# Optimization experiments

Measured on AMD Instinct MI355X. Metric: run time of the kernel, lower is better.

The kernel has to match this reference:

```python
import jax, jax.numpy as jnp
import numpy as np

B, S, D = 2, 2048, 1024
H, DH = 16, 64
INNER = H * DH  # 1024
FF = 4 * D
WINDOW = 128
EPS = 1e-5
SCALE = DH ** -0.5


def setup_inputs() -> dict:
    key = jax.random.key(0)
    ks = jax.random.split(key, 8)
    s = lambda fan_in: 1.0 / np.sqrt(fan_in)
    return {
        "x": jax.random.normal(ks[0], (B, S, D), dtype=jnp.float32),
        "ln1_g": jnp.ones((D,), jnp.float32),
        "ln1_b": jnp.zeros((D,), jnp.float32),
        "w_qkv": jax.random.uniform(ks[1], (3 * INNER, D), jnp.float32, -s(D), s(D)),
        "w_out": jax.random.uniform(ks[2], (D, INNER), jnp.float32, -s(INNER), s(INNER)),
        "b_out": jnp.zeros((D,), jnp.float32),
        "ln2_g": jnp.ones((D,), jnp.float32),
        "ln2_b": jnp.zeros((D,), jnp.float32),
        "w_ff1": jax.random.uniform(ks[3], (FF, D), jnp.float32, -s(D), s(D)),
        "b_ff1": jnp.zeros((FF,), jnp.float32),
        "w_ff2": jax.random.uniform(ks[4], (D, FF), jnp.float32, -s(FF), s(FF)),
        "b_ff2": jnp.zeros((D,), jnp.float32),
    }


def _layernorm(x, g, b):
    mu = jnp.mean(x, axis=-1, keepdims=True)
    var = jnp.mean(jnp.square(x - mu), axis=-1, keepdims=True)
    return (x - mu) * jax.lax.rsqrt(var + EPS) * g + b


def reference(x, ln1_g, ln1_b, w_qkv, w_out, b_out, ln2_g, ln2_b, w_ff1, b_ff1, w_ff2, b_ff2):
    # --- attention block ---
    residual = x
    h = _layernorm(x, ln1_g, ln1_b)
    qkv = h @ w_qkv.T                             # [B, S, 3*INNER]
    q, k, v = jnp.split(qkv, 3, axis=-1)
    reshape_heads = lambda t: t.reshape(B, S, H, DH).transpose(0, 2, 1, 3)  # [B,H,S,DH]
    q, k, v = map(reshape_heads, (q, k, v))
    q = q * SCALE
    scores = jnp.einsum("bhqd,bhkd->bhqk", q, k)  # dense [B,H,S,S]
    # local sparse pattern: attend iff |i-j| <= window_size
    idx = jnp.arange(S)
    local_mask = jnp.abs(idx[:, None] - idx[None, :]) <= WINDOW  # [S,S] bool
    scores = jnp.where(local_mask[None, None], scores, -jnp.inf)
    attn = jax.nn.softmax(scores, axis=-1)
    attn = jnp.nan_to_num(attn, nan=0.0)
    out = jnp.einsum("bhqk,bhkd->bhqd", attn, v)  # [B,H,S,DH]
    out = out.transpose(0, 2, 1, 3).reshape(B, S, INNER)
    out = out @ w_out.T + b_out                   # dropout inactive (eval)
    x = residual + out
    # --- FFN block ---
    residual = x
    h = _layernorm(x, ln2_g, ln2_b)
    h = jax.nn.gelu(h @ w_ff1.T + b_ff1, approximate=False)
    h = h @ w_ff2.T + b_ff2
    return residual + h
```

## Files before the change

### kernel.cpp

```cpp
#include <hip/hip_runtime.h>
#include <stdint.h>

#define SEQ    2048
#define NB     2
#define DMODEL 1024
#define NHEAD  16
#define HDIM   64
#define FFDIM  4096
#define WIN    128
#define MTOK   (NB*SEQ)

typedef short short8 __attribute__((ext_vector_type(8)));
typedef float f32x4  __attribute__((ext_vector_type(4)));

__device__ __forceinline__ float bf2f(uint16_t h){ return __uint_as_float(((uint32_t)h) << 16); }
__device__ __forceinline__ uint16_t f2bf(float f){
  uint32_t u = __float_as_uint(f);
  u += 0x7fffu + ((u >> 16) & 1u);
  return (uint16_t)(u >> 16);
}

__device__ __forceinline__ float gelu_f(float v){
  float u = 0.7978845608028654f * v * (1.0f + 0.044715f * v * v);
  u = fminf(fmaxf(u, -10.0f), 10.0f);
  const float e = __expf(2.0f * u);
  const float th = (e - 1.0f) / (e + 1.0f);
  return 0.5f * v * (1.0f + th);
}

__device__ __forceinline__ void gl_lds16(const void* g, void* l) {
  __builtin_amdgcn_global_load_lds((const __attribute__((address_space(1))) void*)g,
                                   (__attribute__((address_space(3))) void*)l, 16, 0, 0);
}

__global__ __launch_bounds__(256) void cvt4_kernel(
    const float* __restrict__ s0, const float* __restrict__ s1,
    const float* __restrict__ s2, const float* __restrict__ s3,
    uint16_t* __restrict__ d0, uint16_t* __restrict__ d1,
    uint16_t* __restrict__ d2, uint16_t* __restrict__ d3)
{
  size_t i = (size_t)blockIdx.x * 256 + threadIdx.x;
  const float* s; uint16_t* d; size_t off;
  if      (i <  768*1024) { s = s0; d = d0; off = i; }
  else if (i < 1024*1024) { s = s1; d = d1; off = i -  768*1024; }
  else if (i < 2048*1024) { s = s2; d = d2; off = i - 1024*1024; }
  else                    { s = s3; d = d3; off = i - 2048*1024; }
  const float4 v = ((const float4*)s)[off];
  uint2 o;
  o.x = (uint32_t)f2bf(v.x) | ((uint32_t)f2bf(v.y) << 16);
  o.y = (uint32_t)f2bf(v.z) | ((uint32_t)f2bf(v.w) << 16);
  ((uint2*)d)[off] = o;
}

__global__ __launch_bounds__(256) void ln_kernel(const float* __restrict__ x,
                                                 const float* __restrict__ g,
                                                 const float* __restrict__ b,
                                                 uint16_t* __restrict__ y)
{
  const int row = blockIdx.x;
  const int t = threadIdx.x;
  const float4 v = ((const float4*)(x + (size_t)row * DMODEL))[t];
  float s1 = v.x + v.y + v.z + v.w;
  float s2 = v.x*v.x + v.y*v.y + v.z*v.z + v.w*v.w;
  #pragma unroll
  for (int off = 32; off; off >>= 1) { s1 += __shfl_xor(s1, off, 64); s2 += __shfl_xor(s2, off, 64); }
  __shared__ float red[8];
  const int w = t >> 6;
  if ((t & 63) == 0) { red[w] = s1; red[4+w] = s2; }
  __syncthreads();
  s1 = red[0]+red[1]+red[2]+red[3];
  s2 = red[4]+red[5]+red[6]+red[7];
  const float mu = s1 * (1.0f/DMODEL);
  const float var = s2 * (1.0f/DMODEL) - mu*mu;
  const float rs = rsqrtf(var + 1e-5f);
  const float4 gv = ((const float4*)g)[t];
  const float4 bv = ((const float4*)b)[t];
  uint2 o;
  o.x = (uint32_t)f2bf((v.x-mu)*rs*gv.x + bv.x) | ((uint32_t)f2bf((v.y-mu)*rs*gv.y + bv.y) << 16);
  o.y = (uint32_t)f2bf((v.z-mu)*rs*gv.z + bv.z) | ((uint32_t)f2bf((v.w-mu)*rs*gv.w + bv.w) << 16);
  ((uint2*)(y + (size_t)row * DMODEL))[t] = o;
}


template<int EPI>
__global__ __launch_bounds__(256) void gemm_bt(
    const uint16_t* __restrict__ A, const uint16_t* __restrict__ Bm,
    const float* __restrict__ bias, uint16_t* __restrict__ C,
    int M, int N, int K)
{
  __shared__ __align__(16) uint16_t As[128*64];
  __shared__ __align__(16) uint16_t Bs[128*64];
  const int t = threadIdx.x;
  const int l = t & 63;
  const int w = t >> 6;
  const int row0 = blockIdx.y * 128;
  const int col0 = blockIdx.x * 128;
  const int wm = (w >> 1) * 64, wn = (w & 1) * 64;

  f32x4 acc[4][4];
  #pragma unroll
  for (int i = 0; i < 4; ++i)
    #pragma unroll
    for (int j = 0; j < 4; ++j)
      #pragma unroll
      for (int e = 0; e < 4; ++e) acc[i][j][e] = 0.0f;

  const int sr8 = t >> 3;
  const int sg  = (t & 7) ^ (sr8 & 7);
  const uint16_t* aG = A  + (size_t)(row0 + sr8) * K + sg * 8;
  const uint16_t* bG = Bm + (size_t)(col0 + sr8) * K + sg * 8;
  char* aL = (char*)As + t * 16;
  char* bL = (char*)Bs + t * 16;
  const int mrow = l & 15;
  const int kq = l >> 4;

  for (int k0 = 0; k0 < K; k0 += 64) {
    #pragma unroll
    for (int c = 0; c < 4; ++c) {
      gl_lds16(aG + k0 + (size_t)(c*32) * K, aL + c*4096);
      gl_lds16(bG + k0 + (size_t)(c*32) * K, bL + c*4096);
    }
    __syncthreads();
    #pragma unroll
    for (int ks = 0; ks < 2; ++ks) {
      const int pa = ((ks*4 + kq) ^ (mrow & 7)) * 16;
      short8 af[4], bfr[4];
      #pragma unroll
      for (int mi = 0; mi < 4; ++mi)
        af[mi] = *(const short8*)((const char*)As + (wm + mi*16 + mrow) * 128 + pa);
      #pragma unroll
      for (int ni = 0; ni < 4; ++ni)
        bfr[ni] = *(const short8*)((const char*)Bs + (wn + ni*16 + mrow) * 128 + pa);
      #pragma unroll
      for (int mi = 0; mi < 4; ++mi)
        #pragma unroll
        for (int ni = 0; ni < 4; ++ni)
          acc[mi][ni] = __builtin_amdgcn_mfma_f32_16x16x32_bf16(af[mi], bfr[ni], acc[mi][ni], 0, 0, 0);
    }
    __syncthreads();
  }

  const int crow = (l >> 4) * 4;
  float bv[4];
  #pragma unroll
  for (int ni = 0; ni < 4; ++ni)
    bv[ni] = (EPI != 0) ? bias[col0 + wn + ni*16 + mrow] : 0.0f;
  #pragma unroll
  for (int mi = 0; mi < 4; ++mi) {
    #pragma unroll
    for (int r = 0; r < 4; ++r) {
      const int row = row0 + wm + mi*16 + crow + r;
      #pragma unroll
      for (int ni = 0; ni < 4; ++ni) {
        const int col = col0 + wn + ni*16 + mrow;
        float v = acc[mi][ni][r] + bv[ni];
        if (EPI == 2) v = gelu_f(v);
        C[(size_t)row * N + col] = f2bf(v);
      }
    }
  }
}

__global__ __launch_bounds__(256) void gemm_sk64(
    const uint16_t* __restrict__ A, const uint16_t* __restrict__ Bm,
    float* __restrict__ P0, float* __restrict__ P1,
    int M, int N, int K, int KS)
{
  __shared__ __align__(16) uint16_t As[128*64];
  __shared__ __align__(16) uint16_t Bs[64*64];
  const int t = threadIdx.x;
  const int l = t & 63;
  const int w = t >> 6;
  const int row0 = blockIdx.y * 128;
  const int col0 = blockIdx.x * 64;
  const int kbase = blockIdx.z * KS;
  float* P = blockIdx.z ? P1 : P0;
  const int wm = (w >> 1) * 64, wn = (w & 1) * 32;

  f32x4 acc[4][2];
  #pragma unroll
  for (int i = 0; i < 4; ++i)
    #pragma unroll
    for (int j = 0; j < 2; ++j)
      #pragma unroll
      for (int e = 0; e < 4; ++e) acc[i][j][e] = 0.0f;

  const int sr8 = t >> 3;
  const int sg  = (t & 7) ^ (sr8 & 7);
  const uint16_t* aG = A  + (size_t)(row0 + sr8) * K + kbase + sg * 8;
  const uint16_t* bG = Bm + (size_t)(col0 + sr8) * K + kbase + sg * 8;
  char* aL = (char*)As + t * 16;
  char* bL = (char*)Bs + t * 16;
  const int mrow = l & 15;
  const int kq = l >> 4;

  for (int k0 = 0; k0 < KS; k0 += 64) {
    #pragma unroll
    for (int c = 0; c < 4; ++c)
      gl_lds16(aG + k0 + (size_t)(c*32) * K, aL + c*4096);
    #pragma unroll
    for (int c = 0; c < 2; ++c)
      gl_lds16(bG + k0 + (size_t)(c*32) * K, bL + c*4096);
    __syncthreads();
    #pragma unroll
    for (int ks = 0; ks < 2; ++ks) {
      const int pa = ((ks*4 + kq) ^ (mrow & 7)) * 16;
      short8 af[4], bfr[2];
      #pragma unroll
      for (int mi = 0; mi < 4; ++mi)
        af[mi] = *(const short8*)((const char*)As + (wm + mi*16 + mrow) * 128 + pa);
      #pragma unroll
      for (int ni = 0; ni < 2; ++ni)
        bfr[ni] = *(const short8*)((const char*)Bs + (wn + ni*16 + mrow) * 128 + pa);
      #pragma unroll
      for (int mi = 0; mi < 4; ++mi)
        #pragma unroll
        for (int ni = 0; ni < 2; ++ni)
          acc[mi][ni] = __builtin_amdgcn_mfma_f32_16x16x32_bf16(af[mi], bfr[ni], acc[mi][ni], 0, 0, 0);
    }
    __syncthreads();
  }

  const int crow = (l >> 4) * 4;
  #pragma unroll
  for (int mi = 0; mi < 4; ++mi)
    #pragma unroll
    for (int r = 0; r < 4; ++r) {
      const int row = row0 + wm + mi*16 + crow + r;
      #pragma unroll
      for (int ni = 0; ni < 2; ++ni)
        P[(size_t)row * N + col0 + wn + ni*16 + mrow] = acc[mi][ni][r];
    }
}

__global__ __launch_bounds__(256) void gemm_sk128(
    const uint16_t* __restrict__ A, const uint16_t* __restrict__ Bm,
    uint16_t* __restrict__ P0, uint16_t* __restrict__ P1,
    uint16_t* __restrict__ P2, uint16_t* __restrict__ P3,
    int M, int N, int K, int KS)
{
  __shared__ __align__(16) uint16_t As[128*64];
  __shared__ __align__(16) uint16_t Bs[128*64];
  const int t = threadIdx.x;
  const int l = t & 63;
  const int w = t >> 6;
  const int row0 = blockIdx.y * 128;
  const int col0 = blockIdx.x * 128;
  const int z = blockIdx.z;
  const int kbase = z * KS;
  uint16_t* P = (z < 2) ? (z ? P1 : P0) : (z == 2 ? P2 : P3);
  const int wm = (w >> 1) * 64, wn = (w & 1) * 64;

  f32x4 acc[4][4];
  #pragma unroll
  for (int i = 0; i < 4; ++i)
    #pragma unroll
    for (int j = 0; j < 4; ++j)
      #pragma unroll
      for (int e = 0; e < 4; ++e) acc[i][j][e] = 0.0f;

  const int sr8 = t >> 3;
  const int sg  = (t & 7) ^ (sr8 & 7);
  const uint16_t* aG = A  + (size_t)(row0 + sr8) * K + kbase + sg * 8;
  const uint16_t* bG = Bm + (size_t)(col0 + sr8) * K + kbase + sg * 8;
  char* aL = (char*)As + t * 16;
  char* bL = (char*)Bs + t * 16;
  const int mrow = l & 15;
  const int kq = l >> 4;

  for (int k0 = 0; k0 < KS; k0 += 64) {
    #pragma unroll
    for (int c = 0; c < 4; ++c) {
      gl_lds16(aG + k0 + (size_t)(c*32) * K, aL + c*4096);
      gl_lds16(bG + k0 + (size_t)(c*32) * K, bL + c*4096);
    }
    __syncthreads();
    #pragma unroll
    for (int ks = 0; ks < 2; ++ks) {
      const int pa = ((ks*4 + kq) ^ (mrow & 7)) * 16;
      short8 af[4], bfr[4];
      #pragma unroll
      for (int mi = 0; mi < 4; ++mi)
        af[mi] = *(const short8*)((const char*)As + (wm + mi*16 + mrow) * 128 + pa);
      #pragma unroll
      for (int ni = 0; ni < 4; ++ni)
        bfr[ni] = *(const short8*)((const char*)Bs + (wn + ni*16 + mrow) * 128 + pa);
      #pragma unroll
      for (int mi = 0; mi < 4; ++mi)
        #pragma unroll
        for (int ni = 0; ni < 4; ++ni)
          acc[mi][ni] = __builtin_amdgcn_mfma_f32_16x16x32_bf16(af[mi], bfr[ni], acc[mi][ni], 0, 0, 0);
    }
    __syncthreads();
  }

  const int crow = (l >> 4) * 4;
  #pragma unroll
  for (int mi = 0; mi < 4; ++mi)
    #pragma unroll
    for (int r = 0; r < 4; ++r) {
      const int row = row0 + wm + mi*16 + crow + r;
      #pragma unroll
      for (int ni = 0; ni < 4; ++ni)
        P[(size_t)row * N + col0 + wn + ni*16 + mrow] = f2bf(acc[mi][ni][r]);
    }
}

__global__ __launch_bounds__(256) void combine_ln2_kernel(
    const float* __restrict__ p0, const float* __restrict__ p1,
    const float* __restrict__ x,  const float* __restrict__ bout,
    const float* __restrict__ g,  const float* __restrict__ b,
    float* __restrict__ X2f, uint16_t* __restrict__ H2)
{
  const int row = blockIdx.x;
  const int t = threadIdx.x;
  const size_t off = (size_t)row * (DMODEL/4) + t;
  const float4 a0 = ((const float4*)p0)[off];
  const float4 a1 = ((const float4*)p1)[off];
  const float4 xv = ((const float4*)x)[off];
  const float4 bo = ((const float4*)bout)[t];
  float4 v;
  v.x = a0.x + a1.x + xv.x + bo.x;
  v.y = a0.y + a1.y + xv.y + bo.y;
  v.z = a0.z + a1.z + xv.z + bo.z;
  v.w = a0.w + a1.w + xv.w + bo.w;
  ((float4*)X2f)[off] = v;
  float s1 = v.x + v.y + v.z + v.w;
  float s2 = v.x*v.x + v.y*v.y + v.z*v.z + v.w*v.w;
  #pragma unroll
  for (int o = 32; o; o >>= 1) { s1 += __shfl_xor(s1, o, 64); s2 += __shfl_xor(s2, o, 64); }
  __shared__ float red[8];
  const int w = t >> 6;
  if ((t & 63) == 0) { red[w] = s1; red[4+w] = s2; }
  __syncthreads();
  s1 = red[0]+red[1]+red[2]+red[3];
  s2 = red[4]+red[5]+red[6]+red[7];
  const float mu = s1 * (1.0f/DMODEL);
  const float var = s2 * (1.0f/DMODEL) - mu*mu;
  const float rs = rsqrtf(var + 1e-5f);
  const float4 gv = ((const float4*)g)[t];
  const float4 bv = ((const float4*)b)[t];
  uint2 o;
  o.x = (uint32_t)f2bf((v.x-mu)*rs*gv.x + bv.x) | ((uint32_t)f2bf((v.y-mu)*rs*gv.y + bv.y) << 16);
  o.y = (uint32_t)f2bf((v.z-mu)*rs*gv.z + bv.z) | ((uint32_t)f2bf((v.w-mu)*rs*gv.w + bv.w) << 16);
  ((uint2*)(H2 + (size_t)row * DMODEL))[t] = o;
}

__global__ __launch_bounds__(256) void combine_ff2_kernel(
    const uint16_t* __restrict__ p0, const uint16_t* __restrict__ p1,
    const uint16_t* __restrict__ p2, const uint16_t* __restrict__ p3,
    const float* __restrict__ bff2, const float* __restrict__ X2f,
    float* __restrict__ out)
{
  const int row = blockIdx.x;
  const int t = threadIdx.x;
  const size_t eoff = (size_t)row * DMODEL + t * 4;
  const uint2 u0 = *(const uint2*)(p0 + eoff);
  const uint2 u1 = *(const uint2*)(p1 + eoff);
  const uint2 u2 = *(const uint2*)(p2 + eoff);
  const uint2 u3 = *(const uint2*)(p3 + eoff);
  const float4 xv = ((const float4*)X2f)[(size_t)row * (DMODEL/4) + t];
  const float4 bo = ((const float4*)bff2)[t];
  float4 v;
  v.x = bf2f((uint16_t)(u0.x & 0xffff)) + bf2f((uint16_t)(u1.x & 0xffff))
      + bf2f((uint16_t)(u2.x & 0xffff)) + bf2f((uint16_t)(u3.x & 0xffff)) + bo.x + xv.x;
  v.y = bf2f((uint16_t)(u0.x >> 16)) + bf2f((uint16_t)(u1.x >> 16))
      + bf2f((uint16_t)(u2.x >> 16)) + bf2f((uint16_t)(u3.x >> 16)) + bo.y + xv.y;
  v.z = bf2f((uint16_t)(u0.y & 0xffff)) + bf2f((uint16_t)(u1.y & 0xffff))
      + bf2f((uint16_t)(u2.y & 0xffff)) + bf2f((uint16_t)(u3.y & 0xffff)) + bo.z + xv.z;
  v.w = bf2f((uint16_t)(u0.y >> 16)) + bf2f((uint16_t)(u1.y >> 16))
      + bf2f((uint16_t)(u2.y >> 16)) + bf2f((uint16_t)(u3.y >> 16)) + bo.w + xv.w;
  ((float4*)out)[(size_t)row * (DMODEL/4) + t] = v;
}

#define TQ    32
#define NKT   18
#define NKP   (NKT*16)
#define KSTR  72
#define PSTR  296

__global__ __launch_bounds__(256) void attn_kernel(const uint16_t* __restrict__ qkv,
                                                   uint16_t* __restrict__ out)
{
  __shared__ uint16_t Qs[TQ * KSTR];
  __shared__ uint16_t Ps[TQ * PSTR];
  __shared__ uint16_t KV[NKP * KSTR];
  const int t = threadIdx.x, l = t & 63, w = t >> 6;
  const int b = blockIdx.z, hh = blockIdx.y, q0 = blockIdx.x * TQ;
  const int k0 = (q0 - WIN > 0) ? (q0 - WIN) : 0;
  const int kend_ = q0 + TQ + WIN;
  const int kend = (kend_ < SEQ) ? kend_ : SEQ;
  const int nk = kend - k0;

  {
    const int r = t >> 3, gg = t & 7;
    const uint4 qv = *(const uint4*)(qkv + (size_t)(b*SEQ + q0 + r) * 3072 + hh*64 + gg*8);
    *(uint4*)((char*)Qs + r*(KSTR*2) + gg*16) = qv;
    for (int j = r; j < NKP; j += 32) {
      uint4 kv; kv.x = 0; kv.y = 0; kv.z = 0; kv.w = 0;
      if (j < nk)
        kv = *(const uint4*)(qkv + (size_t)(b*SEQ + k0 + j) * 3072 + 1024 + hh*64 + gg*8);
      *(uint4*)((char*)KV + j*(KSTR*2) + gg*16) = kv;
    }
  }
  __syncthreads();

  if (w < 2) {
    const int rb = w * 16;
    const int mrow = l & 15, q4 = l >> 4;
    const short8 aq0 = *(const short8*)((const char*)Qs + (rb + mrow)*(KSTR*2) + q4*16);
    const short8 aq1 = *(const short8*)((const char*)Qs + (rb + mrow)*(KSTR*2) + 64 + q4*16);
    f32x4 cacc[NKT];
    #pragma unroll
    for (int ct = 0; ct < NKT; ++ct) {
      f32x4 c; c[0]=0.f; c[1]=0.f; c[2]=0.f; c[3]=0.f;
      const short8 b0 = *(const short8*)((const char*)KV + (ct*16 + mrow)*(KSTR*2) + q4*16);
      const short8 b1 = *(const short8*)((const char*)KV + (ct*16 + mrow)*(KSTR*2) + 64 + q4*16);
      c = __builtin_amdgcn_mfma_f32_16x16x32_bf16(aq0, b0, c, 0, 0, 0);
      c = __builtin_amdgcn_mfma_f32_16x16x32_bf16(aq1, b1, c, 0, 0, 0);
      cacc[ct] = c;
    }
    #pragma unroll
    for (int r = 0; r < 4; ++r) {
      const int iq = q0 + rb + q4*4 + r;
      float m = -1e30f;
      #pragma unroll
      for (int ct = 0; ct < NKT; ++ct) {
        const int jj = ct*16 + mrow;
        const int j = k0 + jj;
        const bool ok = (jj < nk) && (j >= iq - WIN) && (j <= iq + WIN);
        const float s = ok ? cacc[ct][r] * 0.125f : -1e30f;
        cacc[ct][r] = s;
        m = fmaxf(m, s);
      }
      m = fmaxf(m, __shfl_xor(m, 1, 64));
      m = fmaxf(m, __shfl_xor(m, 2, 64));
      m = fmaxf(m, __shfl_xor(m, 4, 64));
      m = fmaxf(m, __shfl_xor(m, 8, 64));
      float s = 0.f;
      #pragma unroll
      for (int ct = 0; ct < NKT; ++ct) {
        const float e = __expf(cacc[ct][r] - m);
        cacc[ct][r] = e;
        s += e;
      }
      s += __shfl_xor(s, 1, 64);
      s += __shfl_xor(s, 2, 64);
      s += __shfl_xor(s, 4, 64);
      s += __shfl_xor(s, 8, 64);
      const float rinv = 1.0f / s;
      #pragma unroll
      for (int ct = 0; ct < NKT; ++ct)
        Ps[(rb + q4*4 + r) * PSTR + ct*16 + mrow] = f2bf(cacc[ct][r] * rinv);
    }
  }
  __syncthreads();

  {
    uint16_t* Vt = KV;
    const int gg = t & 7;
    for (int j = t >> 3; j < NKP; j += 32) {
      if (j < nk) {
        const uint4 v = *(const uint4*)(qkv + (size_t)(b*SEQ + k0 + j) * 3072 + 2048 + hh*64 + gg*8);
        uint16_t e[8] = { (uint16_t)(v.x & 0xffff), (uint16_t)(v.x >> 16),
                          (uint16_t)(v.y & 0xffff), (uint16_t)(v.y >> 16),
                          (uint16_t)(v.z & 0xffff), (uint16_t)(v.z >> 16),
                          (uint16_t)(v.w & 0xffff), (uint16_t)(v.w >> 16) };
        #pragma unroll
        for (int dd = 0; dd < 8; ++dd) Vt[(gg*8 + dd) * PSTR + j] = e[dd];
      } else {
        #pragma unroll
        for (int dd = 0; dd < 8; ++dd) Vt[(gg*8 + dd) * PSTR + j] = 0;
      }
    }
  }
  __syncthreads();

  {
    const uint16_t* Vt = KV;
    const int mrow = l & 15, q4 = l >> 4;
    const int rt = w & 1, dt0 = (w >> 1) * 2;
    f32x4 o0, o1;
    #pragma unroll
    for (int e = 0; e < 4; ++e) { o0[e] = 0.f; o1[e] = 0.f; }
    #pragma unroll
    for (int ks = 0; ks < 9; ++ks) {
      const short8 a  = *(const short8*)((const char*)Ps + (rt*16 + mrow)*(PSTR*2) + ks*64 + q4*16);
      const short8 v0 = *(const short8*)((const char*)Vt + ((dt0  )*16 + mrow)*(PSTR*2) + ks*64 + q4*16);
      const short8 v1 = *(const short8*)((const char*)Vt + ((dt0+1)*16 + mrow)*(PSTR*2) + ks*64 + q4*16);
      o0 = __builtin_amdgcn_mfma_f32_16x16x32_bf16(a, v0, o0, 0, 0, 0);
      o1 = __builtin_amdgcn_mfma_f32_16x16x32_bf16(a, v1, o1, 0, 0, 0);
    }
    #pragma unroll
    for (int r = 0; r < 4; ++r) {
      const int iq = q0 + rt*16 + q4*4 + r;
      const size_t rowoff = (size_t)(b*SEQ + iq) * DMODEL + hh*64;
      out[rowoff + (dt0  )*16 + mrow] = f2bf(o0[r]);
      out[rowoff + (dt0+1)*16 + mrow] = f2bf(o1[r]);
    }
  }
}

extern "C" void kernel_launch(void* const* d_in, const int* in_sizes, int n_in,
                              void* d_out, int out_size, void* d_ws, size_t ws_size,
                              hipStream_t stream)
{
  const float* x    = (const float*)d_in[0];
  const float* ln1g = (const float*)d_in[1];
  const float* ln1b = (const float*)d_in[2];
  const float* wqkv = (const float*)d_in[3];
  const float* wout = (const float*)d_in[4];
  const float* bout = (const float*)d_in[5];
  const float* ln2g = (const float*)d_in[6];
  const float* ln2b = (const float*)d_in[7];
  const float* wff1 = (const float*)d_in[8];
  const float* bff1 = (const float*)d_in[9];
  const float* wff2 = (const float*)d_in[10];
  const float* bff2 = (const float*)d_in[11];
  float* out = (float*)d_out;

  char* ws = (char*)d_ws;
  const size_t MB = (size_t)1 << 20;
  uint16_t* Wqkv = (uint16_t*)(ws);
  uint16_t* Wout = (uint16_t*)(ws +  6*MB);
  uint16_t* Wff1 = (uint16_t*)(ws +  8*MB);
  uint16_t* Wff2 = (uint16_t*)(ws + 16*MB);
  uint16_t* QKV  = (uint16_t*)(ws + 24*MB);
  uint16_t* H1   = (uint16_t*)(ws + 48*MB);
  uint16_t* AT   = H1;
  float*    X2f  = (float*)   (ws + 56*MB);
  uint16_t* H2   = (uint16_t*)(ws + 72*MB);
  float*    OP0  = (float*)   (ws + 24*MB);
  float*    OP1  = (float*)   (ws + 80*MB);
  uint16_t* FF1  = (uint16_t*)(ws + 24*MB);
  uint16_t* FP0  = (uint16_t*)(ws);
  uint16_t* FP1  = (uint16_t*)(ws +  8*MB);
  uint16_t* FP2  = (uint16_t*)(ws + 72*MB);
  uint16_t* FP3  = (uint16_t*)(ws + 80*MB);

  cvt4_kernel<<<12288, 256, 0, stream>>>(wqkv, wout, wff1, wff2, Wqkv, Wout, Wff1, Wff2);
  ln_kernel<<<MTOK, 256, 0, stream>>>(x, ln1g, ln1b, H1);
  gemm_bt<0><<<dim3(3072/128, MTOK/128), 256, 0, stream>>>(H1, Wqkv, nullptr, QKV, MTOK, 3072, DMODEL);
  attn_kernel<<<dim3(SEQ/TQ, NHEAD, NB), 256, 0, stream>>>(QKV, AT);
  gemm_sk64<<<dim3(DMODEL/64, MTOK/128, 2), 256, 0, stream>>>(AT, Wout, OP0, OP1, MTOK, DMODEL, DMODEL, DMODEL/2);
  combine_ln2_kernel<<<MTOK, 256, 0, stream>>>(OP0, OP1, x, bout, ln2g, ln2b, X2f, H2);
  gemm_bt<2><<<dim3(FFDIM/128, MTOK/128), 256, 0, stream>>>(H2, Wff1, bff1, FF1, MTOK, FFDIM, DMODEL);
  gemm_sk128<<<dim3(DMODEL/128, MTOK/128, 4), 256, 0, stream>>>(FF1, Wff2, FP0, FP1, FP2, FP3, MTOK, DMODEL, FFDIM, FFDIM/4);
  combine_ff2_kernel<<<MTOK, 256, 0, stream>>>(FP0, FP1, FP2, FP3, bff2, X2f, out);
}
```

Baseline: 367.2 us.

## Replace split-K GEMMs with 64x64 tiles and fused bias-residual epilogues

Folds the first layernorm into the weight-conversion kernel so one launch does both. The QKV projection moves to a 128x64 tile GEMM, which gives more blocks. The out-projection and FF2 split-K GEMMs and their combine kernels are replaced by a 64x64-tile GEMM that adds bias and residual directly in its epilogue, removing the partial-sum buffers and the extra passes over them. Layernorm 2 becomes a separate kernel. The trade-off is lower per-block reuse, and the FF2 GEMM now runs the full K=4096 in each block instead of splitting it.

```diff
diff --git a/kernel.cpp b/kernel.cpp
--- a/kernel.cpp
+++ b/kernel.cpp
@@ -33,23 +33,50 @@
                                    (__attribute__((address_space(3))) void*)l, 16, 0, 0);
 }
 
-__global__ __launch_bounds__(256) void cvt4_kernel(
+__global__ __launch_bounds__(256) void cvtln_kernel(
     const float* __restrict__ s0, const float* __restrict__ s1,
     const float* __restrict__ s2, const float* __restrict__ s3,
     uint16_t* __restrict__ d0, uint16_t* __restrict__ d1,
-    uint16_t* __restrict__ d2, uint16_t* __restrict__ d3)
-{
-  size_t i = (size_t)blockIdx.x * 256 + threadIdx.x;
-  const float* s; uint16_t* d; size_t off;
-  if      (i <  768*1024) { s = s0; d = d0; off = i; }
-  else if (i < 1024*1024) { s = s1; d = d1; off = i -  768*1024; }
-  else if (i < 2048*1024) { s = s2; d = d2; off = i - 1024*1024; }
-  else                    { s = s3; d = d3; off = i - 2048*1024; }
-  const float4 v = ((const float4*)s)[off];
-  uint2 o;
-  o.x = (uint32_t)f2bf(v.x) | ((uint32_t)f2bf(v.y) << 16);
-  o.y = (uint32_t)f2bf(v.z) | ((uint32_t)f2bf(v.w) << 16);
-  ((uint2*)d)[off] = o;
+    uint16_t* __restrict__ d2, uint16_t* __restrict__ d3,
+    const float* __restrict__ x, const float* __restrict__ g,
+    const float* __restrict__ b, uint16_t* __restrict__ y)
+{
+  __shared__ float red[8];
+  const int t = threadIdx.x;
+  if (blockIdx.x < 12288) {
+    size_t i = (size_t)blockIdx.x * 256 + t;
+    const float* s; uint16_t* d; size_t off;
+    if      (i <  768*1024) { s = s0; d = d0; off = i; }
+    else if (i < 1024*1024) { s = s1; d = d1; off = i -  768*1024; }
+    else if (i < 2048*1024) { s = s2; d = d2; off = i - 1024*1024; }
+    else                    { s = s3; d = d3; off = i - 2048*1024; }
+    const float4 v = ((const float4*)s)[off];
+    uint2 o;
+    o.x = (uint32_t)f2bf(v.x) | ((uint32_t)f2bf(v.y) << 16);
+    o.y = (uint32_t)f2bf(v.z) | ((uint32_t)f2bf(v.w) << 16);
+    ((uint2*)d)[off] = o;
+  } else {
+    const int row = blockIdx.x - 12288;
+    const float4 v = ((const float4*)(x + (size_t)row * DMODEL))[t];
+    float s1 = v.x + v.y + v.z + v.w;
+    float s2 = v.x*v.x + v.y*v.y + v.z*v.z + v.w*v.w;
+    #pragma unroll
+    for (int off = 32; off; off >>= 1) { s1 += __shfl_xor(s1, off, 64); s2 += __shfl_xor(s2, off, 64); }
+    const int w = t >> 6;
+    if ((t & 63) == 0) { red[w] = s1; red[4+w] = s2; }
+    __syncthreads();
+    s1 = red[0]+red[1]+red[2]+red[3];
+    s2 = red[4]+red[5]+red[6]+red[7];
+    const float mu = s1 * (1.0f/DMODEL);
+    const float var = s2 * (1.0f/DMODEL) - mu*mu;
+    const float rs = rsqrtf(var + 1e-5f);
+    const float4 gv = ((const float4*)g)[t];
+    const float4 bv = ((const float4*)b)[t];
+    uint2 o;
+    o.x = (uint32_t)f2bf((v.x-mu)*rs*gv.x + bv.x) | ((uint32_t)f2bf((v.y-mu)*rs*gv.y + bv.y) << 16);
+    o.y = (uint32_t)f2bf((v.z-mu)*rs*gv.z + bv.z) | ((uint32_t)f2bf((v.w-mu)*rs*gv.w + bv.w) << 16);
+    ((uint2*)(y + (size_t)row * DMODEL))[t] = o;
+  }
 }
 
 __global__ __launch_bounds__(256) void ln_kernel(const float* __restrict__ x,
@@ -161,10 +188,9 @@
   }
 }
 
-__global__ __launch_bounds__(256) void gemm_sk64(
+__global__ __launch_bounds__(256) void gemm_qkv(
     const uint16_t* __restrict__ A, const uint16_t* __restrict__ Bm,
-    float* __restrict__ P0, float* __restrict__ P1,
-    int M, int N, int K, int KS)
+    uint16_t* __restrict__ C, int M, int N, int K)
 {
   __shared__ __align__(16) uint16_t As[128*64];
   __shared__ __align__(16) uint16_t Bs[64*64];
@@ -173,8 +199,6 @@
   const int w = t >> 6;
   const int row0 = blockIdx.y * 128;
   const int col0 = blockIdx.x * 64;
-  const int kbase = blockIdx.z * KS;
-  float* P = blockIdx.z ? P1 : P0;
   const int wm = (w >> 1) * 64, wn = (w & 1) * 32;
 
   f32x4 acc[4][2];
@@ -187,14 +211,14 @@
 
   const int sr8 = t >> 3;
   const int sg  = (t & 7) ^ (sr8 & 7);
-  const uint16_t* aG = A  + (size_t)(row0 + sr8) * K + kbase + sg * 8;
-  const uint16_t* bG = Bm + (size_t)(col0 + sr8) * K + kbase + sg * 8;
+  const uint16_t* aG = A  + (size_t)(row0 + sr8) * K + sg * 8;
+  const uint16_t* bG = Bm + (size_t)(col0 + sr8) * K + sg * 8;
   char* aL = (char*)As + t * 16;
   char* bL = (char*)Bs + t * 16;
   const int mrow = l & 15;
   const int kq = l >> 4;
 
-  for (int k0 = 0; k0 < KS; k0 += 64) {
+  for (int k0 = 0; k0 < K; k0 += 64) {
     #pragma unroll
     for (int c = 0; c < 4; ++c)
       gl_lds16(aG + k0 + (size_t)(c*32) * K, aL + c*4096);
@@ -229,148 +253,82 @@
       const int row = row0 + wm + mi*16 + crow + r;
       #pragma unroll
       for (int ni = 0; ni < 2; ++ni)
-        P[(size_t)row * N + col0 + wn + ni*16 + mrow] = acc[mi][ni][r];
-    }
-}
-
-__global__ __launch_bounds__(256) void gemm_sk128(
+        C[(size_t)row * N + col0 + wn + ni*16 + mrow] = f2bf(acc[mi][ni][r]);
+    }
+}
+
+__global__ __launch_bounds__(256) void gemm64(
     const uint16_t* __restrict__ A, const uint16_t* __restrict__ Bm,
-    uint16_t* __restrict__ P0, uint16_t* __restrict__ P1,
-    uint16_t* __restrict__ P2, uint16_t* __restrict__ P3,
-    int M, int N, int K, int KS)
-{
-  __shared__ __align__(16) uint16_t As[128*64];
-  __shared__ __align__(16) uint16_t Bs[128*64];
+    const float* __restrict__ bias, const float* __restrict__ res,
+    float* __restrict__ out, int M, int N, int K)
+{
+  __shared__ __align__(16) uint16_t As[64*64];
+  __shared__ __align__(16) uint16_t Bs[64*64];
   const int t = threadIdx.x;
   const int l = t & 63;
   const int w = t >> 6;
-  const int row0 = blockIdx.y * 128;
-  const int col0 = blockIdx.x * 128;
-  const int z = blockIdx.z;
-  const int kbase = z * KS;
-  uint16_t* P = (z < 2) ? (z ? P1 : P0) : (z == 2 ? P2 : P3);
-  const int wm = (w >> 1) * 64, wn = (w & 1) * 64;
-
-  f32x4 acc[4][4];
-  #pragma unroll
-  for (int i = 0; i < 4; ++i)
-    #pragma unroll
-    for (int j = 0; j < 4; ++j)
+  const int row0 = blockIdx.y * 64;
+  const int col0 = blockIdx.x * 64;
+  const int wm = (w >> 1) * 32, wn = (w & 1) * 32;
+
+  f32x4 acc[2][2];
+  #pragma unroll
+  for (int i = 0; i < 2; ++i)
+    #pragma unroll
+    for (int j = 0; j < 2; ++j)
       #pragma unroll
       for (int e = 0; e < 4; ++e) acc[i][j][e] = 0.0f;
 
   const int sr8 = t >> 3;
   const int sg  = (t & 7) ^ (sr8 & 7);
-  const uint16_t* aG = A  + (size_t)(row0 + sr8) * K + kbase + sg * 8;
-  const uint16_t* bG = Bm + (size_t)(col0 + sr8) * K + kbase + sg * 8;
+  const uint16_t* aG = A  + (size_t)(row0 + sr8) * K + sg * 8;
+  const uint16_t* bG = Bm + (size_t)(col0 + sr8) * K + sg * 8;
   char* aL = (char*)As + t * 16;
   char* bL = (char*)Bs + t * 16;
   const int mrow = l & 15;
   const int kq = l >> 4;
 
-  for (int k0 = 0; k0 < KS; k0 += 64) {
-    #pragma unroll
-    for (int c = 0; c < 4; ++c) {
-      gl_lds16(aG + k0 + (size_t)(c*32) * K, aL + c*4096);
-      gl_lds16(bG + k0 + (size_t)(c*32) * K, bL + c*4096);
-    }
+  for (int k0 = 0; k0 < K; k0 += 64) {
+    gl_lds16(aG + k0,                    aL);
+    gl_lds16(aG + k0 + (size_t)32 * K,   aL + 4096);
+    gl_lds16(bG + k0,                    bL);
+    gl_lds16(bG + k0 + (size_t)32 * K,   bL + 4096);
     __syncthreads();
     #pragma unroll
     for (int ks = 0; ks < 2; ++ks) {
       const int pa = ((ks*4 + kq) ^ (mrow & 7)) * 16;
-      short8 af[4], bfr[4];
-      #pragma unroll
-      for (int mi = 0; mi < 4; ++mi)
+      short8 af[2], bfr[2];
+      #pragma unroll
+      for (int mi = 0; mi < 2; ++mi)
         af[mi] = *(const short8*)((const char*)As + (wm + mi*16 + mrow) * 128 + pa);
       #pragma unroll
-      for (int ni = 0; ni < 4; ++ni)
+      for (int ni = 0; ni < 2; ++ni)
         bfr[ni] = *(const short8*)((const char*)Bs + (wn + ni*16 + mrow) * 128 + pa);
       #pragma unroll
-      for (int mi = 0; mi < 4; ++mi)
+      for (int mi = 0; mi < 2; ++mi)
         #pragma unroll
-        for (int ni = 0; ni < 4; ++ni)
+        for (int ni = 0; ni < 2; ++ni)
           acc[mi][ni] = __builtin_amdgcn_mfma_f32_16x16x32_bf16(af[mi], bfr[ni], acc[mi][ni], 0, 0, 0);
     }
     __syncthreads();
   }
 
   const int crow = (l >> 4) * 4;
-  #pragma unroll
-  for (int mi = 0; mi < 4; ++mi)
+  float bv[2];
+  #pragma unroll
+  for (int ni = 0; ni < 2; ++ni)
+    bv[ni] = bias[col0 + wn + ni*16 + mrow];
+  #pragma unroll
+  for (int mi = 0; mi < 2; ++mi)
     #pragma unroll
     for (int r = 0; r < 4; ++r) {
       const int row = row0 + wm + mi*16 + crow + r;
       #pragma unroll
-      for (int ni = 0; ni < 4; ++ni)
-        P[(size_t)row * N + col0 + wn + ni*16 + mrow] = f2bf(acc[mi][ni][r]);
-    }
-}
-
-__global__ __launch_bounds__(256) void combine_ln2_kernel(
-    const float* __restrict__ p0, const float* __restrict__ p1,
-    const float* __restrict__ x,  const float* __restrict__ bout,
-    const float* __restrict__ g,  const float* __restrict__ b,
-    float* __restrict__ X2f, uint16_t* __restrict__ H2)
-{
-  const int row = blockIdx.x;
-  const int t = threadIdx.x;
-  const size_t off = (size_t)row * (DMODEL/4) + t;
-  const float4 a0 = ((const float4*)p0)[off];
-  const float4 a1 = ((const float4*)p1)[off];
-  const float4 xv = ((const float4*)x)[off];
-  const float4 bo = ((const float4*)bout)[t];
-  float4 v;
-  v.x = a0.x + a1.x + xv.x + bo.x;
-  v.y = a0.y + a1.y + xv.y + bo.y;
-  v.z = a0.z + a1.z + xv.z + bo.z;
-  v.w = a0.w + a1.w + xv.w + bo.w;
-  ((float4*)X2f)[off] = v;
-  float s1 = v.x + v.y + v.z + v.w;
-  float s2 = v.x*v.x + v.y*v.y + v.z*v.z + v.w*v.w;
-  #pragma unroll
-  for (int o = 32; o; o >>= 1) { s1 += __shfl_xor(s1, o, 64); s2 += __shfl_xor(s2, o, 64); }
-  __shared__ float red[8];
-  const int w = t >> 6;
-  if ((t & 63) == 0) { red[w] = s1; red[4+w] = s2; }
-  __syncthreads();
-  s1 = red[0]+red[1]+red[2]+red[3];
-  s2 = red[4]+red[5]+red[6]+red[7];
-  const float mu = s1 * (1.0f/DMODEL);
-  const float var = s2 * (1.0f/DMODEL) - mu*mu;
-  const float rs = rsqrtf(var + 1e-5f);
-  const float4 gv = ((const float4*)g)[t];
-  const float4 bv = ((const float4*)b)[t];
-  uint2 o;
-  o.x = (uint32_t)f2bf((v.x-mu)*rs*gv.x + bv.x) | ((uint32_t)f2bf((v.y-mu)*rs*gv.y + bv.y) << 16);
-  o.y = (uint32_t)f2bf((v.z-mu)*rs*gv.z + bv.z) | ((uint32_t)f2bf((v.w-mu)*rs*gv.w + bv.w) << 16);
-  ((uint2*)(H2 + (size_t)row * DMODEL))[t] = o;
-}
-
-__global__ __launch_bounds__(256) void combine_ff2_kernel(
-    const uint16_t* __restrict__ p0, const uint16_t* __restrict__ p1,
-    const uint16_t* __restrict__ p2, const uint16_t* __restrict__ p3,
-    const float* __restrict__ bff2, const float* __restrict__ X2f,
-    float* __restrict__ out)
-{
-  const int row = blockIdx.x;
-  const int t = threadIdx.x;
-  const size_t eoff = (size_t)row * DMODEL + t * 4;
-  const uint2 u0 = *(const uint2*)(p0 + eoff);
-  const uint2 u1 = *(const uint2*)(p1 + eoff);
-  const uint2 u2 = *(const uint2*)(p2 + eoff);
-  const uint2 u3 = *(const uint2*)(p3 + eoff);
-  const float4 xv = ((const float4*)X2f)[(size_t)row * (DMODEL/4) + t];
-  const float4 bo = ((const float4*)bff2)[t];
-  float4 v;
-  v.x = bf2f((uint16_t)(u0.x & 0xffff)) + bf2f((uint16_t)(u1.x & 0xffff))
-      + bf2f((uint16_t)(u2.x & 0xffff)) + bf2f((uint16_t)(u3.x & 0xffff)) + bo.x + xv.x;
-  v.y = bf2f((uint16_t)(u0.x >> 16)) + bf2f((uint16_t)(u1.x >> 16))
-      + bf2f((uint16_t)(u2.x >> 16)) + bf2f((uint16_t)(u3.x >> 16)) + bo.y + xv.y;
-  v.z = bf2f((uint16_t)(u0.y & 0xffff)) + bf2f((uint16_t)(u1.y & 0xffff))
-      + bf2f((uint16_t)(u2.y & 0xffff)) + bf2f((uint16_t)(u3.y & 0xffff)) + bo.z + xv.z;
-  v.w = bf2f((uint16_t)(u0.y >> 16)) + bf2f((uint16_t)(u1.y >> 16))
-      + bf2f((uint16_t)(u2.y >> 16)) + bf2f((uint16_t)(u3.y >> 16)) + bo.w + xv.w;
-  ((float4*)out)[(size_t)row * (DMODEL/4) + t] = v;
+      for (int ni = 0; ni < 2; ++ni) {
+        const int col = col0 + wn + ni*16 + mrow;
+        out[(size_t)row * N + col] = acc[mi][ni][r] + bv[ni] + res[(size_t)row * N + col];
+      }
+    }
 }
 
 #define TQ    32
@@ -530,21 +488,15 @@
   uint16_t* AT   = H1;
   float*    X2f  = (float*)   (ws + 56*MB);
   uint16_t* H2   = (uint16_t*)(ws + 72*MB);
-  float*    OP0  = (float*)   (ws + 24*MB);
-  float*    OP1  = (float*)   (ws + 80*MB);
   uint16_t* FF1  = (uint16_t*)(ws + 24*MB);
-  uint16_t* FP0  = (uint16_t*)(ws);
-  uint16_t* FP1  = (uint16_t*)(ws +  8*MB);
-  uint16_t* FP2  = (uint16_t*)(ws + 72*MB);
-  uint16_t* FP3  = (uint16_t*)(ws + 80*MB);
-
-  cvt4_kernel<<<12288, 256, 0, stream>>>(wqkv, wout, wff1, wff2, Wqkv, Wout, Wff1, Wff2);
-  ln_kernel<<<MTOK, 256, 0, stream>>>(x, ln1g, ln1b, H1);
-  gemm_bt<0><<<dim3(3072/128, MTOK/128), 256, 0, stream>>>(H1, Wqkv, nullptr, QKV, MTOK, 3072, DMODEL);
+
+  cvtln_kernel<<<16384, 256, 0, stream>>>(wqkv, wout, wff1, wff2,
+                                          Wqkv, Wout, Wff1, Wff2,
+                                          x, ln1g, ln1b, H1);
+  gemm_qkv<<<dim3(3072/64, MTOK/128), 256, 0, stream>>>(H1, Wqkv, QKV, MTOK, 3072, DMODEL);
   attn_kernel<<<dim3(SEQ/TQ, NHEAD, NB), 256, 0, stream>>>(QKV, AT);
-  gemm_sk64<<<dim3(DMODEL/64, MTOK/128, 2), 256, 0, stream>>>(AT, Wout, OP0, OP1, MTOK, DMODEL, DMODEL, DMODEL/2);
-  combine_ln2_kernel<<<MTOK, 256, 0, stream>>>(OP0, OP1, x, bout, ln2g, ln2b, X2f, H2);
+  gemm64<<<dim3(DMODEL/64, MTOK/64), 256, 0, stream>>>(AT, Wout, bout, x, X2f, MTOK, DMODEL, DMODEL);
+  ln_kernel<<<MTOK, 256, 0, stream>>>(X2f, ln2g, ln2b, H2);
   gemm_bt<2><<<dim3(FFDIM/128, MTOK/128), 256, 0, stream>>>(H2, Wff1, bff1, FF1, MTOK, FFDIM, DMODEL);
-  gemm_sk128<<<dim3(DMODEL/128, MTOK/128, 4), 256, 0, stream>>>(FF1, Wff2, FP0, FP1, FP2, FP3, MTOK, DMODEL, FFDIM, FFDIM/4);
-  combine_ff2_kernel<<<MTOK, 256, 0, stream>>>(FP0, FP1, FP2, FP3, bff2, X2f, out);
-}
+  gemm64<<<dim3(DMODEL/64, MTOK/64), 256, 0, stream>>>(FF1, Wff2, bff2, X2f, out, MTOK, DMODEL, FFDIM);
+}
```

After: 349.8 us. 4.7% less time.
